# Performance work log

Measured on AMD Instinct MI355X. Metric: run time of the kernel, lower is better.

Reference implementation:

```python
import jax, jax.numpy as jnp
import numpy as np

N_U, N_O = 20000, 10000      # rows in users / orders
C = 256                      # channels
TXT = 1536                   # text_embed_dim
NNUM, NCAT, NTXT = 3, 3, 1   # columns per stype (same for both tables)
NCOLS = NNUM + NCAT + NTXT   # 7 columns per table
VOCAB = 101                  # num_cats + 1
E = 10000                    # edges (orders -> users fkey)
MAXP = 16                    # max_parents


def setup_inputs() -> dict:
    key = jax.random.key(0)
    ks = jax.random.split(key, 24)
    s = 0.02
    return {
        "users_num": jax.random.normal(ks[0], (N_U, NNUM), jnp.float32),
        "users_cat": jax.random.randint(ks[1], (N_U, NCAT), 0, VOCAB),
        "users_text": jax.random.normal(ks[2], (N_U, NTXT, TXT), jnp.float32),
        "orders_num": jax.random.normal(ks[3], (N_O, NNUM), jnp.float32),
        "orders_cat": jax.random.randint(ks[4], (N_O, NCAT), 0, VOCAB),
        "orders_text": jax.random.normal(ks[5], (N_O, NTXT, TXT), jnp.float32),
        "edge_index": jax.random.randint(ks[6], (2, E), 0, N_O),
        "table_emb": jax.random.normal(ks[7], (2, C), jnp.float32) * s,
        # users params
        "u_num_w": jax.random.normal(ks[8], (NNUM, C), jnp.float32) * s,
        "u_num_b": jax.random.normal(ks[9], (NNUM, C), jnp.float32) * s,
        "u_cat_tab": jax.random.normal(ks[10], (NCAT, VOCAB, C), jnp.float32) * s,
        "u_txt_w": jax.random.normal(ks[11], (NTXT, C, TXT), jnp.float32) * s,
        "u_txt_b": jax.random.normal(ks[12], (NTXT, C), jnp.float32) * s,
        "u_col": jax.random.normal(ks[13], (NCOLS, C), jnp.float32) * s,
        # orders params
        "o_num_w": jax.random.normal(ks[14], (NNUM, C), jnp.float32) * s,
        "o_num_b": jax.random.normal(ks[15], (NNUM, C), jnp.float32) * s,
        "o_cat_tab": jax.random.normal(ks[16], (NCAT, VOCAB, C), jnp.float32) * s,
        "o_txt_w": jax.random.normal(ks[17], (NTXT, C, TXT), jnp.float32) * s,
        "o_txt_b": jax.random.normal(ks[18], (NTXT, C), jnp.float32) * s,
        "o_col": jax.random.normal(ks[19], (NCOLS, C), jnp.float32) * s,
    }


def _table_tokens(num, cat, txt, nw, nb, ctab, tw, tb, col, temb):
    # num: [N, NNUM]; nw/nb: [NNUM, C] -> per-col Linear(1, C) + SiLU
    tn = jax.nn.silu(num[:, :, None] * nw[None] + nb[None])        # [N, NNUM, C]
    # per-col Embedding lookup: ctab [NCAT, V, C], cat [N, NCAT]
    tc = ctab[jnp.arange(ctab.shape[0])[None, :], cat]             # [N, NCAT, C]
    # per-col Linear(TXT, C): tw [NTXT, C, TXT]
    tt = jnp.einsum('nkt,kct->nkc', txt, tw) + tb[None]            # [N, NTXT, C]
    tok = jnp.concatenate([tn, tc, tt], axis=1) + col[None] + temb  # [N, NCOLS, C]
    # original concatenates per-column blocks of N rows each -> (cols, N, C) flatten
    return tok.transpose(1, 0, 2).reshape(-1, tok.shape[-1])


def reference(users_num, users_cat, users_text, orders_num, orders_cat, orders_text,
              edge_index, table_emb,
              u_num_w, u_num_b, u_cat_tab, u_txt_w, u_txt_b, u_col,
              o_num_w, o_num_b, o_cat_tab, o_txt_w, o_txt_b, o_col):
    xu = _table_tokens(users_num, users_cat, users_text,
                       u_num_w, u_num_b, u_cat_tab, u_txt_w, u_txt_b, u_col, table_emb[0])
    xo = _table_tokens(orders_num, orders_cat, orders_text,
                       o_num_w, o_num_b, o_cat_tab, o_txt_w, o_txt_b, o_col, table_emb[1])
    x = jnp.concatenate([xu, xo], axis=0)                           # [S, C]

    node_idxs = jnp.concatenate([jnp.tile(jnp.arange(N_U), NCOLS),
                                 jnp.tile(jnp.arange(N_U, N_U + N_O), NCOLS)])
    col_idxs = jnp.concatenate([jnp.repeat(jnp.arange(NCOLS), N_U),
                                jnp.repeat(jnp.arange(NCOLS, 2 * NCOLS), N_O)])
    table_idxs = jnp.concatenate([jnp.zeros(NCOLS * N_U, jnp.int32),
                                  jnp.ones(NCOLS * N_O, jnp.int32)])

    # f2p neighbor build: first MAXP parents per child node, in edge order
    num_nodes = N_U + N_O
    child = edge_index[0] + N_U    # orders offset = N_U
    parent = edge_index[1]         # users offset = 0
    order = jnp.argsort(child, stable=True)
    cs, ps = child[order], parent[order]
    seg_start = jnp.searchsorted(cs, cs, side='left')
    rank = jnp.arange(E) - seg_start                                # position within child's group
    valid = rank < MAXP
    tbl = jnp.full((num_nodes + 1, MAXP), -1, dtype=ps.dtype)
    tbl = tbl.at[jnp.where(valid, cs, num_nodes), jnp.minimum(rank, MAXP - 1)].set(
        jnp.where(valid, ps, -1))
    f2p_nbr_idxs = tbl[:num_nodes][node_idxs]                       # [S, MAXP]

    return (x, node_idxs, col_idxs, table_idxs, f2p_nbr_idxs, num_nodes)
```

## Files before the change

kernel.cpp:

```cpp
#include <hip/hip_runtime.h>
#include <hip/hip_bf16.h>

typedef __bf16 bf16;
typedef __bf16 bf16x8 __attribute__((ext_vector_type(8)));
typedef float f32x4 __attribute__((ext_vector_type(4)));

#define NU 20000
#define NO 10000
#define CDIM 256
#define TDIM 1536
#define EN 10000
#define VOCAB 101
#define MAXP 16
#define CAP 32

#define NODE_OFF 53760000LL
#define COL_OFF  53970000LL
#define TAB_OFF  54180000LL
#define F2P_OFF  54390000LL
#define NN_OFF   57750000LL

__global__ void edges_fill(const int* __restrict__ edge, int* __restrict__ counts,
                           unsigned long long* __restrict__ pairs)
{
    int e = blockIdx.x * 256 + threadIdx.x;
    if (e >= EN) return;
    int child = edge[e];
    unsigned parent = (unsigned)edge[EN + e];
    int slot = atomicAdd(&counts[child], 1);
    if (slot < CAP)
        pairs[child * CAP + slot] = ((unsigned long long)(unsigned)e << 32) | parent;
}

__global__ void build_tbl(const int* __restrict__ counts,
                          const unsigned long long* __restrict__ pairs,
                          int* __restrict__ tbl)
{
    int mm = blockIdx.x * 256 + threadIdx.x;
    if (mm >= NO) return;
    int cnt = counts[mm];
    if (cnt > CAP) cnt = CAP;
    unsigned long long v[CAP];
    for (int i = 0; i < cnt; i++) v[i] = pairs[mm * CAP + i];
    for (int i = 1; i < cnt; i++) {
        unsigned long long key = v[i];
        int j = i - 1;
        while (j >= 0 && v[j] > key) { v[j + 1] = v[j]; j--; }
        v[j + 1] = key;
    }
#pragma unroll
    for (int j = 0; j < MAXP; j++)
        tbl[mm * MAXP + j] = (j < cnt) ? (int)(v[j] & 0xffffffffULL) : -1;
}

__global__ __launch_bounds__(256) void idx_f2p(const int* __restrict__ tbl, float* __restrict__ out)
{
    int i = blockIdx.x * 256 + threadIdx.x;
    if (i >= 210000) return;
    float nodev, colvf, tabv;
    int m = -1;
    if (i < 140000) {
        int n = i % 20000;
        nodev = (float)n; colvf = (float)(i / 20000); tabv = 0.f;
    } else {
        int i2 = i - 140000;
        m = i2 % 10000;
        nodev = (float)(20000 + m); colvf = (float)(7 + i2 / 10000); tabv = 1.f;
    }
    out[NODE_OFF + i] = nodev;
    out[COL_OFF + i]  = colvf;
    out[TAB_OFF + i]  = tabv;

    float h[16];
    if (m < 0) {
#pragma unroll
        for (int j = 0; j < 16; j++) h[j] = -1.f;
    } else {
#pragma unroll
        for (int j = 0; j < 16; j++) h[j] = (float)tbl[m * MAXP + j];
    }
    float4* dst = (float4*)&out[F2P_OFF + (long long)i * 16];
#pragma unroll
    for (int j = 0; j < 4; j++)
        dst[j] = *(const float4*)&h[j * 4];
    if (i == 0) out[NN_OFF] = 30000.f;
}

__global__ __launch_bounds__(256) void misc_tokens(
    const float* __restrict__ unum, const int* __restrict__ ucat,
    const float* __restrict__ onum, const int* __restrict__ ocat,
    const float* __restrict__ temb,
    const float* __restrict__ unw, const float* __restrict__ unb,
    const float* __restrict__ uctab, const float* __restrict__ ucol,
    const float* __restrict__ onw, const float* __restrict__ onb,
    const float* __restrict__ octab, const float* __restrict__ ocol,
    float* __restrict__ out)
{
    int t = threadIdx.x;
    int ridx = blockIdx.x * 8 + (t >> 5);
    int c0 = (t & 31) * 8;
    bool isU = ridx < 120000;
    int k, n; long long orow;
    const float *num, *nw, *nb, *ctab, *colw, *te;
    const int* cat;
    if (isU) {
        k = ridx / 20000; n = ridx - k * 20000; orow = ridx;
        num = unum; cat = ucat; nw = unw; nb = unb; ctab = uctab; colw = ucol; te = temb;
    } else {
        int i2 = ridx - 120000;
        k = i2 / 10000; n = i2 - k * 10000; orow = (long long)ridx + 20000;
        num = onum; cat = ocat; nw = onw; nb = onb; ctab = octab; colw = ocol; te = temb + CDIM;
    }
    float colv[8], tev[8];
    *(float4*)&colv[0] = *(const float4*)&colw[k * CDIM + c0];
    *(float4*)&colv[4] = *(const float4*)&colw[k * CDIM + c0 + 4];
    *(float4*)&tev[0]  = *(const float4*)&te[c0];
    *(float4*)&tev[4]  = *(const float4*)&te[c0 + 4];
    float res[8];
    if (k < 3) {
        float v = num[n * 3 + k];
        float wv[8], bv[8];
        *(float4*)&wv[0] = *(const float4*)&nw[k * CDIM + c0];
        *(float4*)&wv[4] = *(const float4*)&nw[k * CDIM + c0 + 4];
        *(float4*)&bv[0] = *(const float4*)&nb[k * CDIM + c0];
        *(float4*)&bv[4] = *(const float4*)&nb[k * CDIM + c0 + 4];
#pragma unroll
        for (int j = 0; j < 8; j++) {
            float x = v * wv[j] + bv[j];
            float s = x / (1.f + __expf(-x));
            res[j] = s + colv[j] + tev[j];
        }
    } else {
        int cv = cat[n * 3 + (k - 3)];
        float tcv[8];
        *(float4*)&tcv[0] = *(const float4*)&ctab[((k - 3) * VOCAB + cv) * CDIM + c0];
        *(float4*)&tcv[4] = *(const float4*)&ctab[((k - 3) * VOCAB + cv) * CDIM + c0 + 4];
#pragma unroll
        for (int j = 0; j < 8; j++)
            res[j] = tcv[j] + colv[j] + tev[j];
    }
    *(float4*)&out[orow * CDIM + c0]     = *(const float4*)&res[0];
    *(float4*)&out[orow * CDIM + c0 + 4] = *(const float4*)&res[4];
}

__global__ __launch_bounds__(256) void gemm_text(
    const float* __restrict__ A, const float* __restrict__ W,
    const float* __restrict__ tbias, const float* __restrict__ colw,
    const float* __restrict__ temb, float* __restrict__ out,
    int M, long long out_row_base)
{
    constexpr int BM = 128, BN = 128, BK = 64, LDA = 72;
    __shared__ bf16 As[BM * LDA];
    __shared__ bf16 Bs[BN * LDA];
    const int tid = threadIdx.x;
    const int m0 = blockIdx.x * BM;
    const int n0 = blockIdx.y * BN;
    const int w = tid >> 6, lane = tid & 63;
    const int wm = (w & 1) * 64, wn = (w >> 1) * 64;
    const int lrow = lane & 15, lquad = lane >> 4;

    f32x4 acc[4][4];
#pragma unroll
    for (int a = 0; a < 4; a++)
#pragma unroll
        for (int b = 0; b < 4; b++) acc[a][b] = (f32x4){0.f, 0.f, 0.f, 0.f};

    for (int k0 = 0; k0 < TDIM; k0 += BK) {
        __syncthreads();
#pragma unroll
        for (int i = 0; i < 8; i++) {
            int c = tid + i * 256;
            int row = c >> 4;
            int col4 = (c & 15) << 2;
            int ga = m0 + row; if (ga >= M) ga = M - 1;
            float4 av = *(const float4*)&A[(size_t)ga * TDIM + k0 + col4];
            __attribute__((aligned(8))) bf16 ha[4] =
                {(bf16)av.x, (bf16)av.y, (bf16)av.z, (bf16)av.w};
            *(unsigned long long*)&As[row * LDA + col4] = *(const unsigned long long*)ha;
            float4 bv = *(const float4*)&W[(size_t)(n0 + row) * TDIM + k0 + col4];
            __attribute__((aligned(8))) bf16 hb[4] =
                {(bf16)bv.x, (bf16)bv.y, (bf16)bv.z, (bf16)bv.w};
            *(unsigned long long*)&Bs[row * LDA + col4] = *(const unsigned long long*)hb;
        }
        __syncthreads();
#pragma unroll
        for (int ks = 0; ks < 2; ks++) {
            bf16x8 afr[4], bfr[4];
#pragma unroll
            for (int mi = 0; mi < 4; mi++)
                afr[mi] = *(const bf16x8*)&As[(wm + mi * 16 + lrow) * LDA + ks * 32 + lquad * 8];
#pragma unroll
            for (int ni = 0; ni < 4; ni++)
                bfr[ni] = *(const bf16x8*)&Bs[(wn + ni * 16 + lrow) * LDA + ks * 32 + lquad * 8];
#pragma unroll
            for (int mi = 0; mi < 4; mi++)
#pragma unroll
                for (int ni = 0; ni < 4; ni++)
                    acc[mi][ni] = __builtin_amdgcn_mfma_f32_16x16x32_bf16(
                        afr[mi], bfr[ni], acc[mi][ni], 0, 0, 0);
        }
    }

#pragma unroll
    for (int ni = 0; ni < 4; ni++) {
        int c = n0 + wn + ni * 16 + lrow;
        float bias = tbias[c] + colw[6 * CDIM + c] + temb[c];
#pragma unroll
        for (int mi = 0; mi < 4; mi++) {
            int mbase = m0 + wm + mi * 16 + lquad * 4;
#pragma unroll
            for (int r = 0; r < 4; r++) {
                int m = mbase + r;
                if (m < M)
                    out[(out_row_base + m) * CDIM + c] = acc[mi][ni][r] + bias;
            }
        }
    }
}

extern "C" void kernel_launch(void* const* d_in, const int* in_sizes, int n_in,
                              void* d_out, int out_size, void* d_ws, size_t ws_size,
                              hipStream_t stream)
{
    const float* users_num   = (const float*)d_in[0];
    const int*   users_cat   = (const int*)d_in[1];
    const float* users_text  = (const float*)d_in[2];
    const float* orders_num  = (const float*)d_in[3];
    const int*   orders_cat  = (const int*)d_in[4];
    const float* orders_text = (const float*)d_in[5];
    const int*   edge_index  = (const int*)d_in[6];
    const float* table_emb   = (const float*)d_in[7];
    const float* u_num_w   = (const float*)d_in[8];
    const float* u_num_b   = (const float*)d_in[9];
    const float* u_cat_tab = (const float*)d_in[10];
    const float* u_txt_w   = (const float*)d_in[11];
    const float* u_txt_b   = (const float*)d_in[12];
    const float* u_col     = (const float*)d_in[13];
    const float* o_num_w   = (const float*)d_in[14];
    const float* o_num_b   = (const float*)d_in[15];
    const float* o_cat_tab = (const float*)d_in[16];
    const float* o_txt_w   = (const float*)d_in[17];
    const float* o_txt_b   = (const float*)d_in[18];
    const float* o_col     = (const float*)d_in[19];
    float* out = (float*)d_out;

    int* counts = (int*)d_ws;
    unsigned long long* pairs = (unsigned long long*)((char*)d_ws + 65536);
    int* tbl = (int*)((char*)d_ws + 65536 + (size_t)NO * CAP * 8);

    hipMemsetAsync(counts, 0, NO * sizeof(int), stream);
    edges_fill<<<(EN + 255) / 256, 256, 0, stream>>>(edge_index, counts, pairs);
    build_tbl<<<(NO + 255) / 256, 256, 0, stream>>>(counts, pairs, tbl);
    idx_f2p<<<(210000 + 255) / 256, 256, 0, stream>>>(tbl, out);
    misc_tokens<<<22500, 256, 0, stream>>>(users_num, users_cat, orders_num, orders_cat,
        table_emb, u_num_w, u_num_b, u_cat_tab, u_col,
        o_num_w, o_num_b, o_cat_tab, o_col, out);
    gemm_text<<<dim3(157, 2), 256, 0, stream>>>(users_text, u_txt_w, u_txt_b, u_col,
        table_emb, out, NU, 120000LL);
    gemm_text<<<dim3(79, 2), 256, 0, stream>>>(orders_text, o_txt_w, o_txt_b, o_col,
        table_emb + CDIM, out, NO, 200000LL);
}
```

Measured before the change: 503.4 us.

## Merge GEMM, misc-token and index kernels into one heterogeneous launch

```diff
diff --git a/kernel.cpp b/kernel.cpp
--- a/kernel.cpp
+++ b/kernel.cpp
@@ -19,6 +19,14 @@
 #define TAB_OFF  54180000LL
 #define F2P_OFF  54390000LL
 #define NN_OFF   57750000LL
+
+#define GEMM_U_BLKS 314
+#define GEMM_O_BLKS 158
+#define MISC_BLKS   22500
+#define IDX_BLKS    840
+#define MISC_OFF    (GEMM_U_BLKS + GEMM_O_BLKS)
+#define IDX_OFF     (MISC_OFF + MISC_BLKS)
+#define TOTAL_BLKS  (IDX_OFF + IDX_BLKS)
 
 __global__ void edges_fill(const int* __restrict__ edge, int* __restrict__ counts,
                            unsigned long long* __restrict__ pairs)
@@ -53,9 +61,10 @@
         tbl[mm * MAXP + j] = (j < cnt) ? (int)(v[j] & 0xffffffffULL) : -1;
 }
 
-__global__ __launch_bounds__(256) void idx_f2p(const int* __restrict__ tbl, float* __restrict__ out)
-{
-    int i = blockIdx.x * 256 + threadIdx.x;
+__device__ __forceinline__ void idx_body(int iblk, const int* __restrict__ tbl,
+                                         float* __restrict__ out)
+{
+    int i = iblk * 256 + threadIdx.x;
     if (i >= 210000) return;
     float nodev, colvf, tabv;
     int m = -1;
@@ -86,7 +95,7 @@
     if (i == 0) out[NN_OFF] = 30000.f;
 }
 
-__global__ __launch_bounds__(256) void misc_tokens(
+__device__ __forceinline__ void misc_body(int mb,
     const float* __restrict__ unum, const int* __restrict__ ucat,
     const float* __restrict__ onum, const int* __restrict__ ocat,
     const float* __restrict__ temb,
@@ -97,7 +106,7 @@
     float* __restrict__ out)
 {
     int t = threadIdx.x;
-    int ridx = blockIdx.x * 8 + (t >> 5);
+    int ridx = mb * 8 + (t >> 5);
     int c0 = (t & 31) * 8;
     bool isU = ridx < 120000;
     int k, n; long long orow;
@@ -143,18 +152,17 @@
     *(float4*)&out[orow * CDIM + c0 + 4] = *(const float4*)&res[4];
 }
 
-__global__ __launch_bounds__(256) void gemm_text(
+__device__ __forceinline__ void gemm_body(
     const float* __restrict__ A, const float* __restrict__ W,
     const float* __restrict__ tbias, const float* __restrict__ colw,
     const float* __restrict__ temb, float* __restrict__ out,
-    int M, long long out_row_base)
-{
-    constexpr int BM = 128, BN = 128, BK = 64, LDA = 72;
-    __shared__ bf16 As[BM * LDA];
-    __shared__ bf16 Bs[BN * LDA];
+    int M, long long out_row_base, int mblk, int nblk,
+    bf16* As, bf16* Bs)
+{
+    constexpr int BK = 64, LDA = 72;
     const int tid = threadIdx.x;
-    const int m0 = blockIdx.x * BM;
-    const int n0 = blockIdx.y * BN;
+    const int m0 = mblk * 128;
+    const int n0 = nblk * 128;
     const int w = tid >> 6, lane = tid & 63;
     const int wm = (w & 1) * 64, wn = (w >> 1) * 64;
     const int lrow = lane & 15, lquad = lane >> 4;
@@ -215,6 +223,38 @@
                     out[(out_row_base + m) * CDIM + c] = acc[mi][ni][r] + bias;
             }
         }
+    }
+}
+
+__global__ __launch_bounds__(256) void mega(
+    const float* __restrict__ users_num, const int* __restrict__ users_cat,
+    const float* __restrict__ users_text,
+    const float* __restrict__ orders_num, const int* __restrict__ orders_cat,
+    const float* __restrict__ orders_text,
+    const float* __restrict__ temb,
+    const float* __restrict__ unw, const float* __restrict__ unb,
+    const float* __restrict__ uctab, const float* __restrict__ utw,
+    const float* __restrict__ utb, const float* __restrict__ ucol,
+    const float* __restrict__ onw, const float* __restrict__ onb,
+    const float* __restrict__ octab, const float* __restrict__ otw,
+    const float* __restrict__ otb, const float* __restrict__ ocol,
+    const int* __restrict__ tbl, float* __restrict__ out)
+{
+    __shared__ bf16 As[128 * 72];
+    __shared__ bf16 Bs[128 * 72];
+    int b = blockIdx.x;
+    if (b < GEMM_U_BLKS) {
+        gemm_body(users_text, utw, utb, ucol, temb, out,
+                  NU, 120000LL, b >> 1, b & 1, As, Bs);
+    } else if (b < MISC_OFF) {
+        int bb = b - GEMM_U_BLKS;
+        gemm_body(orders_text, otw, otb, ocol, temb + CDIM, out,
+                  NO, 200000LL, bb >> 1, bb & 1, As, Bs);
+    } else if (b < IDX_OFF) {
+        misc_body(b - MISC_OFF, users_num, users_cat, orders_num, orders_cat,
+                  temb, unw, unb, uctab, ucol, onw, onb, octab, ocol, out);
+    } else {
+        idx_body(b - IDX_OFF, tbl, out);
     }
 }
 
@@ -251,12 +291,8 @@
     hipMemsetAsync(counts, 0, NO * sizeof(int), stream);
     edges_fill<<<(EN + 255) / 256, 256, 0, stream>>>(edge_index, counts, pairs);
     build_tbl<<<(NO + 255) / 256, 256, 0, stream>>>(counts, pairs, tbl);
-    idx_f2p<<<(210000 + 255) / 256, 256, 0, stream>>>(tbl, out);
-    misc_tokens<<<22500, 256, 0, stream>>>(users_num, users_cat, orders_num, orders_cat,
-        table_emb, u_num_w, u_num_b, u_cat_tab, u_col,
-        o_num_w, o_num_b, o_cat_tab, o_col, out);
-    gemm_text<<<dim3(157, 2), 256, 0, stream>>>(users_text, u_txt_w, u_txt_b, u_col,
-        table_emb, out, NU, 120000LL);
-    gemm_text<<<dim3(79, 2), 256, 0, stream>>>(orders_text, o_txt_w, o_txt_b, o_col,
-        table_emb + CDIM, out, NO, 200000LL);
-}
+    mega<<<TOTAL_BLKS, 256, 0, stream>>>(
+        users_num, users_cat, users_text, orders_num, orders_cat, orders_text,
+        table_emb, u_num_w, u_num_b, u_cat_tab, u_txt_w, u_txt_b, u_col,
+        o_num_w, o_num_b, o_cat_tab, o_txt_w, o_txt_b, o_col, tbl, out);
+}
```

After: 479.6 us. 1.05x faster.
